# Performance work log

Measured on AMD Instinct MI355X. Metric: run time of the kernel, lower is better.

## Reference

```python
import jax, jax.numpy as jnp
import numpy as np

NUM_ITER = 5
DIM = 512
BATCH = 64


def setup_inputs() -> dict:
    key = jax.random.key(0)
    a = jax.random.normal(key, (BATCH, DIM, DIM), dtype=jnp.float32)
    # Symmetric PSD input (covariance-like), as in bilinear pooling; Newton-Schulz
    # requires SPD matrices for convergence.
    x = jnp.einsum('bik,bjk->bij', a, a) / DIM
    I = jnp.eye(DIM, dtype=jnp.float32)
    return {"x": x, "I": I}


def reference(x, I):
    # x: [bs, dim, dim]; I: [dim, dim]
    normA = jnp.sqrt(jnp.sum(x * x, axis=(1, 2), keepdims=True))  # Frobenius norm per matrix
    Y = x / normA
    bs, dim, _ = x.shape
    Z = jnp.broadcast_to(I, (bs, dim, dim))
    Ib = Z
    for _ in range(NUM_ITER):
        T = 0.5 * (3.0 * Ib - jnp.matmul(Z, Y))
        Y = jnp.matmul(Y, T)
        Z = jnp.matmul(T, Z)
    sA = Y * jnp.sqrt(normA)
    return sA
```

## Files before the change

kernel.cpp:

```cpp
#include <hip/hip_runtime.h>
#include <hip/hip_bf16.h>
#include <stdint.h>

#define DIM   512
#define BATCH 64
#define KENC  1024
#define BM    256
#define BN    256
#define BKT   32
#define NKT   16
#define BUFE  32768

typedef __attribute__((ext_vector_type(8))) short short8;
typedef __attribute__((ext_vector_type(4))) float floatx4;

__device__ __forceinline__ ushort f2bf(float f) {
    __hip_bfloat16 h = __float2bfloat16(f);
    return *(ushort*)&h;
}
__device__ __forceinline__ float bf2f(ushort u) {
    __hip_bfloat16 h = *(__hip_bfloat16*)&u;
    return (float)h;
}

typedef __attribute__((address_space(3))) uint32_t lds_u32;
typedef const __attribute__((address_space(1))) uint32_t glb_u32;
__device__ __forceinline__ void gload16(const ushort* g, ushort* l) {
    __builtin_amdgcn_global_load_lds((glb_u32*)g, (lds_u32*)l, 16, 0, 0);
}

#define WAITVM(N) asm volatile("s_waitcnt vmcnt(" #N ")" ::: "memory")
#define BARRIER() do { __builtin_amdgcn_s_barrier(); __builtin_amdgcn_sched_barrier(0); } while (0)
#define SCHED()   __builtin_amdgcn_sched_barrier(0)

__global__ __launch_bounds__(256) void norm_partial_kernel(const float* __restrict__ x,
                                                           float* __restrict__ partial) {
    int b = blockIdx.y;
    int i = blockIdx.x;
    const float4* xv = (const float4*)(x + (size_t)b * DIM * DIM + (size_t)i * (DIM * DIM / 16));
    float s = 0.f;
    #pragma unroll
    for (int r = 0; r < 16; ++r) {
        float4 v = xv[r * 256 + threadIdx.x];
        s += v.x * v.x + v.y * v.y + v.z * v.z + v.w * v.w;
    }
    #pragma unroll
    for (int off = 32; off > 0; off >>= 1) s += __shfl_down(s, off, 64);
    __shared__ float red[4];
    int lane = threadIdx.x & 63, wid = threadIdx.x >> 6;
    if (lane == 0) red[wid] = s;
    __syncthreads();
    if (threadIdx.x == 0) partial[b * 16 + i] = red[0] + red[1] + red[2] + red[3];
}

__global__ __launch_bounds__(256) void init_kernel(const float* __restrict__ x,
                                                   const float* __restrict__ partial,
                                                   float* __restrict__ norms,
                                                   ushort* __restrict__ Yenc,
                                                   ushort* __restrict__ Tenc) {
    int b = blockIdx.y;
    float s = 0.f;
    #pragma unroll
    for (int p = 0; p < 16; ++p) s += partial[b * 16 + p];
    float nrm = sqrtf(s);
    if (blockIdx.x == 0 && threadIdx.x == 0) norms[b] = nrm;
    float inv = 1.0f / nrm;
    int idx = (blockIdx.x * 256 + threadIdx.x) * 4;
    int r = idx >> 9;
    int c = idx & 511;
    float4 v = *(const float4*)(x + (size_t)b * DIM * DIM + idx);
    float yv[4] = {v.x * inv, v.y * inv, v.z * inv, v.w * inv};
    size_t base = (size_t)b * DIM * KENC + (size_t)r * KENC;
    ushort yhi[4], ylo[4], thi[4], tlo[4];
    #pragma unroll
    for (int j = 0; j < 4; ++j) {
        float y = yv[j];
        yhi[j] = f2bf(y);
        ylo[j] = f2bf(y - bf2f(yhi[j]));
        float t = ((c + j) == r ? 1.5f : 0.0f) - 0.5f * y;
        thi[j] = f2bf(t);
        tlo[j] = f2bf(t - bf2f(thi[j]));
    }
    *(ushort4*)(Yenc + base + c)       = *(ushort4*)yhi;
    *(ushort4*)(Yenc + base + 512 + c) = *(ushort4*)ylo;
    *(ushort4*)(Tenc + base + c)       = *(ushort4*)thi;
    *(ushort4*)(Tenc + base + 512 + c) = *(ushort4*)tlo;
}

__device__ __forceinline__ void stage_hi(ushort* buf, const ushort* Ag, const ushort* Bg,
                                         int k0, int tid) {
    #pragma unroll
    for (int s = 0; s < 2; ++s) {
        int vt = tid + s * 512;
        int row = vt >> 2;
        int pc  = vt & 3;
        int kc  = ((pc ^ ((row >> 1) & 3)) << 3);
        const ushort* ar = Ag + (size_t)row * KENC + k0 + kc;
        const ushort* br = Bg + (size_t)row * KENC + k0 + kc;
        gload16(ar, &buf[vt * 8]);
        gload16(br, &buf[16384 + vt * 8]);
    }
}
__device__ __forceinline__ void stage_lo(ushort* buf, const ushort* Ag, const ushort* Bg,
                                         int k0, int tid) {
    #pragma unroll
    for (int s = 0; s < 2; ++s) {
        int vt = tid + s * 512;
        int row = vt >> 2;
        int pc  = vt & 3;
        int kc  = ((pc ^ ((row >> 1) & 3)) << 3);
        const ushort* ar = Ag + (size_t)row * KENC + k0 + kc;
        const ushort* br = Bg + (size_t)row * KENC + k0 + kc;
        gload16(ar + 512, &buf[8192 + vt * 8]);
        gload16(br + 512, &buf[24576 + vt * 8]);
    }
}

__device__ __forceinline__ void store_enc(ushort* Cenc, size_t matoff, int gr, int gc, float v) {
    ushort hi = f2bf(v);
    ushort lo = f2bf(v - bf2f(hi));
    Cenc[matoff + (size_t)gr * KENC + gc] = hi;
    Cenc[matoff + (size_t)gr * KENC + 512 + gc] = lo;
}

template <int MODE>
__global__ __launch_bounds__(512, 2) void gemm_bt(const ushort* __restrict__ A,
                                                  const ushort* __restrict__ B,
                                                  ushort* __restrict__ Cenc,
                                                  float* __restrict__ Cout,
                                                  const float* __restrict__ norms) {
    __shared__ __attribute__((aligned(16))) ushort sm[2 * BUFE];

    int f = blockIdx.x;
    int xcd = f & 7;
    int g   = f >> 3;
    int b   = xcd + 8 * (g >> 2);
    int t   = g & 3;
    int bm  = t >> 1;
    int bn  = t & 1;

    size_t matoff = (size_t)b * DIM * KENC;
    const ushort* Ag = A + matoff + (size_t)bm * BM * KENC;
    const ushort* Bg = B + matoff + (size_t)bn * BN * KENC;

    int tid = threadIdx.x;
    int wave = tid >> 6, lane = tid & 63;
    int lane15 = lane & 15, quad = lane >> 4;
    int wrow = (wave >> 2) * 128;
    int wcol = (wave & 3) * 64;
    int s2 = (lane15 >> 1) & 3;
    int fo = ((quad ^ s2) << 3);

    floatx4 acc[8][4];
    #pragma unroll
    for (int i = 0; i < 8; ++i)
        #pragma unroll
        for (int j = 0; j < 4; ++j)
            acc[i][j] = (floatx4){0.f, 0.f, 0.f, 0.f};

    stage_hi(sm, Ag, Bg, 0, tid);
    stage_lo(sm, Ag, Bg, 0, tid);

    #pragma unroll 2
    for (int kt = 0; kt < NKT; ++kt) {
        const ushort* cur = sm + (kt & 1) * BUFE;
        ushort* nxt = sm + ((kt + 1) & 1) * BUFE;
        const ushort* Ash = cur;
        const ushort* Asl = cur + 8192;
        const ushort* Bsh = cur + 16384;
        const ushort* Bsl = cur + 24576;

        short8 ah[8], bh[4], bl[4], al[4];

        WAITVM(4);
        BARRIER();

        #pragma unroll
        for (int i = 0; i < 4; ++i)
            ah[i] = *(const short8*)&Ash[(wrow + i * 16 + lane15) * BKT + fo];
        #pragma unroll
        for (int j = 0; j < 4; ++j)
            bh[j] = *(const short8*)&Bsh[(wcol + j * 16 + lane15) * BKT + fo];
        if (kt + 1 < NKT) stage_hi(nxt, Ag, Bg, (kt + 1) * BKT, tid);
        __builtin_amdgcn_s_setprio(1);
        #pragma unroll
        for (int i = 0; i < 4; ++i)
            #pragma unroll
            for (int j = 0; j < 4; ++j)
                acc[i][j] = __builtin_amdgcn_mfma_f32_16x16x32_bf16(ah[i], bh[j], acc[i][j], 0, 0, 0);
        __builtin_amdgcn_s_setprio(0);
        SCHED();

        #pragma unroll
        for (int i = 4; i < 8; ++i)
            ah[i] = *(const short8*)&Ash[(wrow + i * 16 + lane15) * BKT + fo];
        __builtin_amdgcn_s_setprio(1);
        #pragma unroll
        for (int i = 4; i < 8; ++i)
            #pragma unroll
            for (int j = 0; j < 4; ++j)
                acc[i][j] = __builtin_amdgcn_mfma_f32_16x16x32_bf16(ah[i], bh[j], acc[i][j], 0, 0, 0);
        __builtin_amdgcn_s_setprio(0);
        SCHED();

        if (kt + 1 < NKT) { WAITVM(4); }
        else             { WAITVM(0); }
        BARRIER();

        #pragma unroll
        for (int j = 0; j < 4; ++j)
            bl[j] = *(const short8*)&Bsl[(wcol + j * 16 + lane15) * BKT + fo];
        if (kt + 1 < NKT) stage_lo(nxt, Ag, Bg, (kt + 1) * BKT, tid);
        __builtin_amdgcn_s_setprio(1);
        #pragma unroll
        for (int i = 0; i < 4; ++i)
            #pragma unroll
            for (int j = 0; j < 4; ++j)
                acc[i][j] = __builtin_amdgcn_mfma_f32_16x16x32_bf16(ah[i], bl[j], acc[i][j], 0, 0, 0);
        __builtin_amdgcn_s_setprio(0);
        SCHED();

        __builtin_amdgcn_s_setprio(1);
        #pragma unroll
        for (int i = 4; i < 8; ++i)
            #pragma unroll
            for (int j = 0; j < 4; ++j)
                acc[i][j] = __builtin_amdgcn_mfma_f32_16x16x32_bf16(ah[i], bl[j], acc[i][j], 0, 0, 0);
        __builtin_amdgcn_s_setprio(0);
        SCHED();

        #pragma unroll
        for (int i = 0; i < 4; ++i)
            al[i] = *(const short8*)&Asl[(wrow + i * 16 + lane15) * BKT + fo];
        __builtin_amdgcn_s_setprio(1);
        #pragma unroll
        for (int i = 0; i < 4; ++i)
            #pragma unroll
            for (int j = 0; j < 4; ++j)
                acc[i][j] = __builtin_amdgcn_mfma_f32_16x16x32_bf16(al[i], bh[j], acc[i][j], 0, 0, 0);
        __builtin_amdgcn_s_setprio(0);
        SCHED();

        #pragma unroll
        for (int i = 0; i < 4; ++i)
            al[i] = *(const short8*)&Asl[(wrow + (i + 4) * 16 + lane15) * BKT + fo];
        __builtin_amdgcn_s_setprio(1);
        #pragma unroll
        for (int i = 0; i < 4; ++i)
            #pragma unroll
            for (int j = 0; j < 4; ++j)
                acc[i + 4][j] = __builtin_amdgcn_mfma_f32_16x16x32_bf16(al[i], bh[j], acc[i + 4][j], 0, 0, 0);
        __builtin_amdgcn_s_setprio(0);
        SCHED();
    }

    float scale = (MODE == 2) ? sqrtf(norms[b]) : 0.f;
    #pragma unroll
    for (int i = 0; i < 8; ++i) {
        int gr0 = bm * BM + wrow + i * 16 + quad * 4;
        #pragma unroll
        for (int j = 0; j < 4; ++j) {
            int gc = bn * BN + wcol + j * 16 + lane15;
            #pragma unroll
            for (int rr = 0; rr < 4; ++rr) {
                int gr = gr0 + rr;
                float cv = acc[i][j][rr];
                if (MODE == 0) {
                    store_enc(Cenc, matoff, gr, gc, (gr == gc ? 1.5f : 0.0f) - 0.5f * cv);
                } else if (MODE == 1) {
                    store_enc(Cenc, matoff, gr, gc, cv);
                } else {
                    Cout[(size_t)b * DIM * DIM + (size_t)gr * DIM + gc] = cv * scale;
                }
            }
        }
    }
}

extern "C" void kernel_launch(void* const* d_in, const int* in_sizes, int n_in,
                              void* d_out, int out_size, void* d_ws, size_t ws_size,
                              hipStream_t stream) {
    const float* x = (const float*)d_in[0];
    float* out = (float*)d_out;

    const size_t MATB = (size_t)BATCH * DIM * KENC * sizeof(ushort);
    char* ws = (char*)d_ws;
    ushort* W0 = (ushort*)(ws + 0 * MATB);
    ushort* W1 = (ushort*)(ws + 1 * MATB);
    ushort* W2 = (ushort*)(ws + 2 * MATB);
    float* partial = (float*)(ws + 3 * MATB);
    float* norms   = (float*)(ws + 3 * MATB + 4096);
    ushort* D = (ushort*)d_out;

    dim3 gblk(512);
    dim3 g1(256);

    norm_partial_kernel<<<dim3(16, BATCH), 256, 0, stream>>>(x, partial);
    init_kernel<<<dim3(256, BATCH), 256, 0, stream>>>(x, partial, norms, W0, W1);

    gemm_bt<1><<<g1, gblk, 0, stream>>>(W0, W1, W2, nullptr, nullptr);
    gemm_bt<0><<<g1, gblk, 0, stream>>>(W1, W2, W0, nullptr, nullptr);
    gemm_bt<1><<<g1, gblk, 0, stream>>>(W2, W0, D, nullptr, nullptr);
    gemm_bt<1><<<g1, gblk, 0, stream>>>(W0, W1, W2, nullptr, nullptr);
    gemm_bt<0><<<g1, gblk, 0, stream>>>(W2, D, W0, nullptr, nullptr);
    gemm_bt<1><<<g1, gblk, 0, stream>>>(D, W0, W1, nullptr, nullptr);
    gemm_bt<1><<<g1, gblk, 0, stream>>>(W0, W2, D, nullptr, nullptr);
    gemm_bt<0><<<g1, gblk, 0, stream>>>(D, W1, W0, nullptr, nullptr);
    gemm_bt<1><<<g1, gblk, 0, stream>>>(W1, W0, W2, nullptr, nullptr);
    gemm_bt<1><<<g1, gblk, 0, stream>>>(W0, D, W1, nullptr, nullptr);
    gemm_bt<0><<<g1, gblk, 0, stream>>>(W1, W2, W0, nullptr, nullptr);
    gemm_bt<2><<<g1, gblk, 0, stream>>>(W2, W0, nullptr, out, norms);
}
```

Baseline: 715.8 us.

## Software-pipeline LDS fragment loads so each read overlaps the previous MFMA group

Restructures the K-loop of the split-bf16 GEMM so every LDS fragment load is issued one MFMA group ahead of its use. The first A-hi and B-hi fragments of the next k-tile are prefetched at the end of the current iteration, and the MFMA groups are reordered so the loads of a47, b_l, l03 and l47 sit in the shadow of earlier math. This targets LDS latency stalls between barriers. It costs more live VGPRs for the extra fragment registers, which may reduce occupancy, and it moves a barrier into the tail of the loop.

```diff
diff --git a/kernel.cpp b/kernel.cpp
--- a/kernel.cpp
+++ b/kernel.cpp
@@ -160,6 +160,16 @@
 
     stage_hi(sm, Ag, Bg, 0, tid);
     stage_lo(sm, Ag, Bg, 0, tid);
+    WAITVM(4);
+    BARRIER();
+
+    short8 a03[4], b_h[4];
+    #pragma unroll
+    for (int i = 0; i < 4; ++i)
+        a03[i] = *(const short8*)&sm[(wrow + i * 16 + lane15) * BKT + fo];
+    #pragma unroll
+    for (int j = 0; j < 4; ++j)
+        b_h[j] = *(const short8*)&sm[16384 + (wcol + j * 16 + lane15) * BKT + fo];
 
     #pragma unroll 2
     for (int kt = 0; kt < NKT; ++kt) {
@@ -170,88 +180,101 @@
         const ushort* Bsh = cur + 16384;
         const ushort* Bsl = cur + 24576;
 
-        short8 ah[8], bh[4], bl[4], al[4];
-
-        WAITVM(4);
-        BARRIER();
-
-        #pragma unroll
-        for (int i = 0; i < 4; ++i)
-            ah[i] = *(const short8*)&Ash[(wrow + i * 16 + lane15) * BKT + fo];
-        #pragma unroll
-        for (int j = 0; j < 4; ++j)
-            bh[j] = *(const short8*)&Bsh[(wcol + j * 16 + lane15) * BKT + fo];
+        short8 a47[4], b_l[4], l03[4], l47[4], na[4], nb[4];
+
+        #pragma unroll
+        for (int i = 0; i < 4; ++i)
+            a47[i] = *(const short8*)&Ash[(wrow + (i + 4) * 16 + lane15) * BKT + fo];
         if (kt + 1 < NKT) stage_hi(nxt, Ag, Bg, (kt + 1) * BKT, tid);
-        __builtin_amdgcn_s_setprio(1);
-        #pragma unroll
-        for (int i = 0; i < 4; ++i)
-            #pragma unroll
-            for (int j = 0; j < 4; ++j)
-                acc[i][j] = __builtin_amdgcn_mfma_f32_16x16x32_bf16(ah[i], bh[j], acc[i][j], 0, 0, 0);
-        __builtin_amdgcn_s_setprio(0);
-        SCHED();
-
-        #pragma unroll
-        for (int i = 4; i < 8; ++i)
-            ah[i] = *(const short8*)&Ash[(wrow + i * 16 + lane15) * BKT + fo];
-        __builtin_amdgcn_s_setprio(1);
-        #pragma unroll
-        for (int i = 4; i < 8; ++i)
-            #pragma unroll
-            for (int j = 0; j < 4; ++j)
-                acc[i][j] = __builtin_amdgcn_mfma_f32_16x16x32_bf16(ah[i], bh[j], acc[i][j], 0, 0, 0);
+        SCHED();
+        __builtin_amdgcn_s_setprio(1);
+        #pragma unroll
+        for (int i = 0; i < 4; ++i)
+            #pragma unroll
+            for (int j = 0; j < 4; ++j)
+                acc[i][j] = __builtin_amdgcn_mfma_f32_16x16x32_bf16(a03[i], b_h[j], acc[i][j], 0, 0, 0);
         __builtin_amdgcn_s_setprio(0);
         SCHED();
 
         if (kt + 1 < NKT) { WAITVM(4); }
         else             { WAITVM(0); }
         BARRIER();
-
         #pragma unroll
         for (int j = 0; j < 4; ++j)
-            bl[j] = *(const short8*)&Bsl[(wcol + j * 16 + lane15) * BKT + fo];
+            b_l[j] = *(const short8*)&Bsl[(wcol + j * 16 + lane15) * BKT + fo];
+        SCHED();
+        __builtin_amdgcn_s_setprio(1);
+        #pragma unroll
+        for (int i = 0; i < 4; ++i)
+            #pragma unroll
+            for (int j = 0; j < 4; ++j)
+                acc[i + 4][j] = __builtin_amdgcn_mfma_f32_16x16x32_bf16(a47[i], b_h[j], acc[i + 4][j], 0, 0, 0);
+        __builtin_amdgcn_s_setprio(0);
+        SCHED();
+
+        #pragma unroll
+        for (int i = 0; i < 4; ++i)
+            l03[i] = *(const short8*)&Asl[(wrow + i * 16 + lane15) * BKT + fo];
         if (kt + 1 < NKT) stage_lo(nxt, Ag, Bg, (kt + 1) * BKT, tid);
-        __builtin_amdgcn_s_setprio(1);
-        #pragma unroll
-        for (int i = 0; i < 4; ++i)
-            #pragma unroll
-            for (int j = 0; j < 4; ++j)
-                acc[i][j] = __builtin_amdgcn_mfma_f32_16x16x32_bf16(ah[i], bl[j], acc[i][j], 0, 0, 0);
-        __builtin_amdgcn_s_setprio(0);
-        SCHED();
-
-        __builtin_amdgcn_s_setprio(1);
-        #pragma unroll
-        for (int i = 4; i < 8; ++i)
-            #pragma unroll
-            for (int j = 0; j < 4; ++j)
-                acc[i][j] = __builtin_amdgcn_mfma_f32_16x16x32_bf16(ah[i], bl[j], acc[i][j], 0, 0, 0);
-        __builtin_amdgcn_s_setprio(0);
-        SCHED();
-
-        #pragma unroll
-        for (int i = 0; i < 4; ++i)
-            al[i] = *(const short8*)&Asl[(wrow + i * 16 + lane15) * BKT + fo];
-        __builtin_amdgcn_s_setprio(1);
-        #pragma unroll
-        for (int i = 0; i < 4; ++i)
-            #pragma unroll
-            for (int j = 0; j < 4; ++j)
-                acc[i][j] = __builtin_amdgcn_mfma_f32_16x16x32_bf16(al[i], bh[j], acc[i][j], 0, 0, 0);
-        __builtin_amdgcn_s_setprio(0);
-        SCHED();
-
-        #pragma unroll
-        for (int i = 0; i < 4; ++i)
-            al[i] = *(const short8*)&Asl[(wrow + (i + 4) * 16 + lane15) * BKT + fo];
-        __builtin_amdgcn_s_setprio(1);
-        #pragma unroll
-        for (int i = 0; i < 4; ++i)
-            #pragma unroll
-            for (int j = 0; j < 4; ++j)
-                acc[i + 4][j] = __builtin_amdgcn_mfma_f32_16x16x32_bf16(al[i], bh[j], acc[i + 4][j], 0, 0, 0);
-        __builtin_amdgcn_s_setprio(0);
-        SCHED();
+        SCHED();
+        __builtin_amdgcn_s_setprio(1);
+        #pragma unroll
+        for (int i = 0; i < 4; ++i)
+            #pragma unroll
+            for (int j = 0; j < 4; ++j)
+                acc[i][j] = __builtin_amdgcn_mfma_f32_16x16x32_bf16(a03[i], b_l[j], acc[i][j], 0, 0, 0);
+        __builtin_amdgcn_s_setprio(0);
+        SCHED();
+
+        #pragma unroll
+        for (int i = 0; i < 4; ++i)
+            l47[i] = *(const short8*)&Asl[(wrow + (i + 4) * 16 + lane15) * BKT + fo];
+        SCHED();
+        __builtin_amdgcn_s_setprio(1);
+        #pragma unroll
+        for (int i = 0; i < 4; ++i)
+            #pragma unroll
+            for (int j = 0; j < 4; ++j)
+                acc[i + 4][j] = __builtin_amdgcn_mfma_f32_16x16x32_bf16(a47[i], b_l[j], acc[i + 4][j], 0, 0, 0);
+        __builtin_amdgcn_s_setprio(0);
+        SCHED();
+
+        if (kt + 1 < NKT) {
+            WAITVM(4);
+            BARRIER();
+            #pragma unroll
+            for (int j = 0; j < 4; ++j)
+                nb[j] = *(const short8*)&nxt[16384 + (wcol + j * 16 + lane15) * BKT + fo];
+        }
+        SCHED();
+        __builtin_amdgcn_s_setprio(1);
+        #pragma unroll
+        for (int i = 0; i < 4; ++i)
+            #pragma unroll
+            for (int j = 0; j < 4; ++j)
+                acc[i][j] = __builtin_amdgcn_mfma_f32_16x16x32_bf16(l03[i], b_h[j], acc[i][j], 0, 0, 0);
+        __builtin_amdgcn_s_setprio(0);
+        SCHED();
+
+        if (kt + 1 < NKT) {
+            #pragma unroll
+            for (int i = 0; i < 4; ++i)
+                na[i] = *(const short8*)&nxt[(wrow + i * 16 + lane15) * BKT + fo];
+        }
+        SCHED();
+        __builtin_amdgcn_s_setprio(1);
+        #pragma unroll
+        for (int i = 0; i < 4; ++i)
+            #pragma unroll
+            for (int j = 0; j < 4; ++j)
+                acc[i + 4][j] = __builtin_amdgcn_mfma_f32_16x16x32_bf16(l47[i], b_h[j], acc[i + 4][j], 0, 0, 0);
+        __builtin_amdgcn_s_setprio(0);
+        SCHED();
+
+        if (kt + 1 < NKT) {
+            #pragma unroll
+            for (int i = 0; i < 4; ++i) { a03[i] = na[i]; b_h[i] = nb[i]; }
+        }
     }
 
     float scale = (MODE == 2) ? sqrtf(norms[b]) : 0.f;
```

Measured after the change: 1.201 ms. 67.8% more time.

## Split tile prefetch into four planes interleaved with MFMA phases using workgroup barriers

Applied to the files above, without the earlier changes.

Replaces the two-stage hi/lo prefetch with four per-plane loads (A-hi, B-hi, A-lo, B-lo), each issued between MFMA phases of the current k-tile. Sched barriers become full workgroup barriers around each phase so the waves run MFMA clusters in lockstep, a ping-pong style schedule. The vmcnt waits move to the end of each iteration, and the loop is no longer unrolled by 2. The intent is to spread global-to-LDS traffic evenly across the compute, at the cost of many more s_barrier syncs per k-step.

```diff
diff --git a/kernel.cpp b/kernel.cpp
--- a/kernel.cpp
+++ b/kernel.cpp
@@ -31,7 +31,6 @@
 
 #define WAITVM(N) asm volatile("s_waitcnt vmcnt(" #N ")" ::: "memory")
 #define BARRIER() do { __builtin_amdgcn_s_barrier(); __builtin_amdgcn_sched_barrier(0); } while (0)
-#define SCHED()   __builtin_amdgcn_sched_barrier(0)
 
 __global__ __launch_bounds__(256) void norm_partial_kernel(const float* __restrict__ x,
                                                            float* __restrict__ partial) {
@@ -87,32 +86,14 @@
     *(ushort4*)(Tenc + base + 512 + c) = *(ushort4*)tlo;
 }
 
-__device__ __forceinline__ void stage_hi(ushort* buf, const ushort* Ag, const ushort* Bg,
-                                         int k0, int tid) {
+__device__ __forceinline__ void stage_plane(ushort* dst, const ushort* src, int k0, int tid) {
     #pragma unroll
     for (int s = 0; s < 2; ++s) {
         int vt = tid + s * 512;
         int row = vt >> 2;
         int pc  = vt & 3;
         int kc  = ((pc ^ ((row >> 1) & 3)) << 3);
-        const ushort* ar = Ag + (size_t)row * KENC + k0 + kc;
-        const ushort* br = Bg + (size_t)row * KENC + k0 + kc;
-        gload16(ar, &buf[vt * 8]);
-        gload16(br, &buf[16384 + vt * 8]);
-    }
-}
-__device__ __forceinline__ void stage_lo(ushort* buf, const ushort* Ag, const ushort* Bg,
-                                         int k0, int tid) {
-    #pragma unroll
-    for (int s = 0; s < 2; ++s) {
-        int vt = tid + s * 512;
-        int row = vt >> 2;
-        int pc  = vt & 3;
-        int kc  = ((pc ^ ((row >> 1) & 3)) << 3);
-        const ushort* ar = Ag + (size_t)row * KENC + k0 + kc;
-        const ushort* br = Bg + (size_t)row * KENC + k0 + kc;
-        gload16(ar + 512, &buf[8192 + vt * 8]);
-        gload16(br + 512, &buf[24576 + vt * 8]);
+        gload16(src + (size_t)row * KENC + k0 + kc, &dst[vt * 8]);
     }
 }
 
@@ -158,10 +139,13 @@
         for (int j = 0; j < 4; ++j)
             acc[i][j] = (floatx4){0.f, 0.f, 0.f, 0.f};
 
-    stage_hi(sm, Ag, Bg, 0, tid);
-    stage_lo(sm, Ag, Bg, 0, tid);
-
-    #pragma unroll 2
+    stage_plane(sm,         Ag,       0, tid);
+    stage_plane(sm + 16384, Bg,       0, tid);
+    stage_plane(sm + 8192,  Ag + 512, 0, tid);
+    stage_plane(sm + 24576, Bg + 512, 0, tid);
+    WAITVM(4);
+    BARRIER();
+
     for (int kt = 0; kt < NKT; ++kt) {
         const ushort* cur = sm + (kt & 1) * BUFE;
         ushort* nxt = sm + ((kt + 1) & 1) * BUFE;
@@ -169,69 +153,72 @@
         const ushort* Asl = cur + 8192;
         const ushort* Bsh = cur + 16384;
         const ushort* Bsl = cur + 24576;
-
-        short8 ah[8], bh[4], bl[4], al[4];
-
-        WAITVM(4);
-        BARRIER();
-
-        #pragma unroll
-        for (int i = 0; i < 4; ++i)
-            ah[i] = *(const short8*)&Ash[(wrow + i * 16 + lane15) * BKT + fo];
+        int k1 = (kt + 1) * BKT;
+        bool pre = (kt + 1 < NKT);
+
+        short8 ah03[4], ah47[4], bh[4], bl[4], al[4];
+
+        #pragma unroll
+        for (int i = 0; i < 4; ++i)
+            ah03[i] = *(const short8*)&Ash[(wrow + i * 16 + lane15) * BKT + fo];
         #pragma unroll
         for (int j = 0; j < 4; ++j)
             bh[j] = *(const short8*)&Bsh[(wcol + j * 16 + lane15) * BKT + fo];
-        if (kt + 1 < NKT) stage_hi(nxt, Ag, Bg, (kt + 1) * BKT, tid);
-        __builtin_amdgcn_s_setprio(1);
-        #pragma unroll
-        for (int i = 0; i < 4; ++i)
-            #pragma unroll
-            for (int j = 0; j < 4; ++j)
-                acc[i][j] = __builtin_amdgcn_mfma_f32_16x16x32_bf16(ah[i], bh[j], acc[i][j], 0, 0, 0);
-        __builtin_amdgcn_s_setprio(0);
-        SCHED();
-
-        #pragma unroll
-        for (int i = 4; i < 8; ++i)
-            ah[i] = *(const short8*)&Ash[(wrow + i * 16 + lane15) * BKT + fo];
-        __builtin_amdgcn_s_setprio(1);
-        #pragma unroll
-        for (int i = 4; i < 8; ++i)
-            #pragma unroll
-            for (int j = 0; j < 4; ++j)
-                acc[i][j] = __builtin_amdgcn_mfma_f32_16x16x32_bf16(ah[i], bh[j], acc[i][j], 0, 0, 0);
-        __builtin_amdgcn_s_setprio(0);
-        SCHED();
-
-        if (kt + 1 < NKT) { WAITVM(4); }
-        else             { WAITVM(0); }
+        if (pre) stage_plane(nxt, Ag, k1, tid);
+        BARRIER();
+        __builtin_amdgcn_s_setprio(1);
+        #pragma unroll
+        for (int i = 0; i < 4; ++i)
+            #pragma unroll
+            for (int j = 0; j < 4; ++j)
+                acc[i][j] = __builtin_amdgcn_mfma_f32_16x16x32_bf16(ah03[i], bh[j], acc[i][j], 0, 0, 0);
+        __builtin_amdgcn_s_setprio(0);
+        BARRIER();
+
+        #pragma unroll
+        for (int i = 0; i < 4; ++i)
+            ah47[i] = *(const short8*)&Ash[(wrow + (i + 4) * 16 + lane15) * BKT + fo];
+        if (pre) stage_plane(nxt + 16384, Bg, k1, tid);
+        BARRIER();
+        __builtin_amdgcn_s_setprio(1);
+        #pragma unroll
+        for (int i = 0; i < 4; ++i)
+            #pragma unroll
+            for (int j = 0; j < 4; ++j)
+                acc[i + 4][j] = __builtin_amdgcn_mfma_f32_16x16x32_bf16(ah47[i], bh[j], acc[i + 4][j], 0, 0, 0);
+        __builtin_amdgcn_s_setprio(0);
+        if (pre) { WAITVM(4); } else { WAITVM(0); }
         BARRIER();
 
         #pragma unroll
         for (int j = 0; j < 4; ++j)
             bl[j] = *(const short8*)&Bsl[(wcol + j * 16 + lane15) * BKT + fo];
-        if (kt + 1 < NKT) stage_lo(nxt, Ag, Bg, (kt + 1) * BKT, tid);
-        __builtin_amdgcn_s_setprio(1);
-        #pragma unroll
-        for (int i = 0; i < 4; ++i)
-            #pragma unroll
-            for (int j = 0; j < 4; ++j)
-                acc[i][j] = __builtin_amdgcn_mfma_f32_16x16x32_bf16(ah[i], bl[j], acc[i][j], 0, 0, 0);
-        __builtin_amdgcn_s_setprio(0);
-        SCHED();
-
-        __builtin_amdgcn_s_setprio(1);
-        #pragma unroll
-        for (int i = 4; i < 8; ++i)
-            #pragma unroll
-            for (int j = 0; j < 4; ++j)
-                acc[i][j] = __builtin_amdgcn_mfma_f32_16x16x32_bf16(ah[i], bl[j], acc[i][j], 0, 0, 0);
-        __builtin_amdgcn_s_setprio(0);
-        SCHED();
+        if (pre) stage_plane(nxt + 8192, Ag + 512, k1, tid);
+        BARRIER();
+        __builtin_amdgcn_s_setprio(1);
+        #pragma unroll
+        for (int i = 0; i < 4; ++i)
+            #pragma unroll
+            for (int j = 0; j < 4; ++j)
+                acc[i][j] = __builtin_amdgcn_mfma_f32_16x16x32_bf16(ah03[i], bl[j], acc[i][j], 0, 0, 0);
+        __builtin_amdgcn_s_setprio(0);
+        BARRIER();
+
+        if (pre) stage_plane(nxt + 24576, Bg + 512, k1, tid);
+        BARRIER();
+        __builtin_amdgcn_s_setprio(1);
+        #pragma unroll
+        for (int i = 0; i < 4; ++i)
+            #pragma unroll
+            for (int j = 0; j < 4; ++j)
+                acc[i + 4][j] = __builtin_amdgcn_mfma_f32_16x16x32_bf16(ah47[i], bl[j], acc[i + 4][j], 0, 0, 0);
+        __builtin_amdgcn_s_setprio(0);
+        BARRIER();
 
         #pragma unroll
         for (int i = 0; i < 4; ++i)
             al[i] = *(const short8*)&Asl[(wrow + i * 16 + lane15) * BKT + fo];
+        BARRIER();
         __builtin_amdgcn_s_setprio(1);
         #pragma unroll
         for (int i = 0; i < 4; ++i)
@@ -239,11 +226,12 @@
             for (int j = 0; j < 4; ++j)
                 acc[i][j] = __builtin_amdgcn_mfma_f32_16x16x32_bf16(al[i], bh[j], acc[i][j], 0, 0, 0);
         __builtin_amdgcn_s_setprio(0);
-        SCHED();
+        BARRIER();
 
         #pragma unroll
         for (int i = 0; i < 4; ++i)
             al[i] = *(const short8*)&Asl[(wrow + (i + 4) * 16 + lane15) * BKT + fo];
+        BARRIER();
         __builtin_amdgcn_s_setprio(1);
         #pragma unroll
         for (int i = 0; i < 4; ++i)
@@ -251,7 +239,8 @@
             for (int j = 0; j < 4; ++j)
                 acc[i + 4][j] = __builtin_amdgcn_mfma_f32_16x16x32_bf16(al[i], bh[j], acc[i + 4][j], 0, 0, 0);
         __builtin_amdgcn_s_setprio(0);
-        SCHED();
+        if (pre) WAITVM(4);
+        BARRIER();
     }
 
     float scale = (MODE == 2) ? sqrtf(norms[b]) : 0.f;
```

Result: slower. 765.6 us (+7.0%).
